# Kernel optimization log

Hardware: AMD Instinct MI355X
Metric: run time of the kernel (lower is better)

The kernel has to match this reference:

```python
import jax, jax.numpy as jnp
import numpy as np

D_MODEL = 2048
D_FF = 8192
EPS = 1e-5


def layernorm(x, g, b):
    m = x.mean(-1, keepdims=True)
    v = ((x - m) ** 2).mean(-1, keepdims=True)
    return (x - m) * jax.lax.rsqrt(v + EPS) * g + b


def rotate_half(x):
    return jnp.concatenate([-x[..., ::2], x[..., 1::2]], axis=-1)


def sinu_pos_emb(dim, length):
    inv_freq = 1.0 / 10000 ** (jnp.arange(0, dim, 2, dtype=jnp.float32) / dim)
    pos = jnp.arange(length, dtype=jnp.float32)
    sp = pos[:, None] * inv_freq[None, :]           # [S, dim/2]
    return jnp.concatenate([jnp.sin(sp), jnp.cos(sp)], axis=-1)  # [S, dim]


def setup_inputs() -> dict:
    key = jax.random.key(0)
    ks = jax.random.split(key, 10)
    d, f = D_MODEL, D_FF
    sc = 0.02
    return {
        "src":  jax.random.normal(ks[0], (4, 2048, d), jnp.float32),
        "Wqkv": jax.random.normal(ks[1], (3 * d, d), jnp.float32) * sc,
        "bqkv": jnp.zeros((3 * d,), jnp.float32),
        "Wo":   jax.random.normal(ks[2], (d, d), jnp.float32) * sc,
        "bo":   jnp.zeros((d,), jnp.float32),
        "W1":   jax.random.normal(ks[3], (f, d), jnp.float32) * sc,
        "b1":   jnp.zeros((f,), jnp.float32),
        "W2":   jax.random.normal(ks[4], (d, f), jnp.float32) * sc,
        "b2":   jnp.zeros((d,), jnp.float32),
        "g1":   jnp.ones((d,), jnp.float32),
        "be1":  jnp.zeros((d,), jnp.float32),
        "g2":   jnp.ones((d,), jnp.float32),
        "be2":  jnp.zeros((d,), jnp.float32),
    }


def reference(src, Wqkv, bqkv, Wo, bo, W1, b1, W2, b2, g1, be1, g2, be2):
    B, S, d = src.shape
    # norm1 (note: torch code reassigns src, so residuals use the normed value)
    src = layernorm(src, g1, be1)
    qkv = src @ Wqkv.T + bqkv                      # [B,S,3d]
    Q, K, V = qkv[..., :d], qkv[..., d:2 * d], qkv[..., 2 * d:]
    # rotary: cos/sin of the (sin,cos)-concatenated table, faithful to source
    emb = sinu_pos_emb(d, S)                       # [S,d]
    c, s = jnp.cos(emb), jnp.sin(emb)
    Q = Q * c + rotate_half(Q) * s
    K = K * c - rotate_half(K) * s
    # causal SDPA over full d_model (no head split in source)
    scale = 1.0 / jnp.sqrt(jnp.float32(d))
    scores = jnp.einsum('bqd,bkd->bqk', Q, K) * scale
    causal = jnp.tril(jnp.ones((S, S), bool))
    scores = jnp.where(causal, scores, jnp.float32(-1e30))
    P = jax.nn.softmax(scores, axis=-1)
    attn = jnp.einsum('bqk,bkd->bqd', P, V)
    src = src + attn @ Wo.T + bo
    # FFN block
    h = layernorm(src, g2, be2)
    h = jax.nn.relu(h @ W1.T + b1) @ W2.T + b2
    return src + h
```

## Files before the change

kernel.cpp:

```cpp
#include <hip/hip_runtime.h>
#include <cstdint>


typedef __attribute__((ext_vector_type(8))) short short8;
typedef __attribute__((ext_vector_type(4))) float floatx4;

#define PLANE 16777216L
#define SS    4194304L

__device__ __forceinline__ float bf2f(unsigned short u) {
    union { unsigned int i; float f; } v; v.i = ((unsigned int)u) << 16; return v.f;
}
__device__ __forceinline__ unsigned short f2bf(float f) {
    union { float f; unsigned int i; } v; v.f = f;
    unsigned int x = v.i;
    return (unsigned short)((x + 0x7FFFu + ((x >> 16) & 1u)) >> 16);
}
__device__ __forceinline__ uint4 pack8(float4 a, float4 b) {
    unsigned short o[8];
    o[0] = f2bf(a.x); o[1] = f2bf(a.y); o[2] = f2bf(a.z); o[3] = f2bf(a.w);
    o[4] = f2bf(b.x); o[5] = f2bf(b.y); o[6] = f2bf(b.z); o[7] = f2bf(b.w);
    return *(uint4*)o;
}
__device__ __forceinline__ void gl_lds16(const void* g, void* l) {
    __builtin_amdgcn_global_load_lds(
        (const __attribute__((address_space(1))) void*)g,
        (__attribute__((address_space(3))) void*)l, 16, 0, 0);
}

#define EM_QKV  0
#define EM_SC   1
#define EM_PV   2
#define EM_PROJ 3
#define EM_FFN1 4
#define EM_F2A  5

template<int EM>
__launch_bounds__(256, 2)
__global__ void gemm_bt(const unsigned short* __restrict__ A,
                        const unsigned short* __restrict__ B,
                        void* __restrict__ Cv, int N, int K,
                        const float* __restrict__ bias,
                        const unsigned short* __restrict__ resid16,
                        unsigned short* __restrict__ outQ,
                        unsigned short* __restrict__ outVt)
{
    constexpr int BM = 128, BN = 128, BK = 32;
    __shared__ __align__(16) unsigned short As[BM * BK];
    __shared__ __align__(16) unsigned short Bs[BN * BK];

    const int m0 = blockIdx.x * BM, n0 = blockIdx.y * BN;
    if (EM == EM_SC && n0 > m0 + (BM - 1)) return;

    int kmax = K;
    if (EM == EM_PV) { kmax = m0 + BM; if (kmax > K) kmax = K; }
    const int nsteps = kmax / BK;

    const int t = threadIdx.x;
    const int lane = t & 63, wave = t >> 6;
    const int q = lane >> 4, ln = lane & 15;
    const int wm = (wave >> 1) * 64, wn = (wave & 1) * 64;

    const int r0 = wave * 32;
    const int rA = r0 + (lane >> 2);
    const int cslot = lane & 3;
    const int cg0 = (cslot ^ (rA & 3)) * 8;
    const int cg1 = (cslot ^ ((rA + 16) & 3)) * 8;
    const unsigned short* Agp0 = A + (long)(m0 + rA) * K + cg0;
    const unsigned short* Agp1 = A + (long)(m0 + rA + 16) * K + cg1;
    const unsigned short* Bgp0 = B + (long)(n0 + rA) * K + cg0;
    const unsigned short* Bgp1 = B + (long)(n0 + rA + 16) * K + cg1;
    unsigned short* lA0 = &As[r0 * 32];
    unsigned short* lA1 = &As[(r0 + 16) * 32];
    unsigned short* lB0 = &Bs[r0 * 32];
    unsigned short* lB1 = &Bs[(r0 + 16) * 32];

    floatx4 acc[4][4];
#pragma unroll
    for (int i = 0; i < 4; ++i)
#pragma unroll
        for (int j = 0; j < 4; ++j) acc[i][j] = (floatx4){0.f, 0.f, 0.f, 0.f};

    for (int s = 0; s < nsteps; ++s) {
        const long off = (long)s * BK;
        __syncthreads();
        gl_lds16(Agp0 + off, lA0);
        gl_lds16(Agp1 + off, lA1);
        gl_lds16(Bgp0 + off, lB0);
        gl_lds16(Bgp1 + off, lB1);
        __syncthreads();
        short8 af[4], bfr[4];
#pragma unroll
        for (int i = 0; i < 4; ++i) {
            const int R = wm + 16 * i + ln;
            af[i] = *(const short8*)&As[R * 32 + ((q ^ (R & 3)) * 8)];
        }
#pragma unroll
        for (int j = 0; j < 4; ++j) {
            const int R = wn + 16 * j + ln;
            bfr[j] = *(const short8*)&Bs[R * 32 + ((q ^ (R & 3)) * 8)];
        }
#pragma unroll
        for (int i = 0; i < 4; ++i)
#pragma unroll
            for (int j = 0; j < 4; ++j)
                acc[i][j] = __builtin_amdgcn_mfma_f32_16x16x32_bf16(af[i], bfr[j], acc[i][j], 0, 0, 0);
    }

#pragma unroll
    for (int i = 0; i < 4; ++i) {
#pragma unroll
        for (int r = 0; r < 4; ++r) {
            const int row = m0 + wm + 16 * i + q * 4 + r;
#pragma unroll
            for (int j = 0; j < 4; ++j) {
                const int col = n0 + wn + 16 * j + ln;
                float v = acc[i][j][r];
                const long idx = (long)row * N + col;
                if constexpr (EM == EM_SC) {
                    ((unsigned short*)Cv)[idx] = f2bf(v);
                } else if constexpr (EM == EM_PV) {
                    ((unsigned short*)Cv)[idx] = f2bf(v);
                }
            }
        }
    }
}

#define BAR()    __builtin_amdgcn_s_barrier()
#define LGKM0()  asm volatile("s_waitcnt lgkmcnt(0)" ::: "memory")
#define VMCNT(n) asm volatile("s_waitcnt vmcnt(" #n ")" ::: "memory")

template<int EM>
__launch_bounds__(512, 2)
__global__ void gemm256(const unsigned short* __restrict__ A,
                        const unsigned short* __restrict__ B,
                        void* __restrict__ Cv, int N, int K,
                        const float* __restrict__ bias,
                        const unsigned short* __restrict__ resid16,
                        unsigned short* __restrict__ outQ,
                        unsigned short* __restrict__ outVt)
{
    __shared__ __align__(16) unsigned short As[2][16384];
    __shared__ __align__(16) unsigned short Bs[2][16384];

    const int m0 = blockIdx.x * 256, n0 = blockIdx.y * 256;
    const int t = threadIdx.x;
    const int lane = t & 63, wave = t >> 6;
    const int q = lane >> 4, ln = lane & 15;
    const int wm = wave >> 2, wn = wave & 3;

    const int jrow = lane >> 3;
    const int csrc = ((lane & 7) ^ jrow) * 8;
    const unsigned short* Ag = A + (long)(m0 + wave * 16 + jrow) * K + csrc;
    const unsigned short* Bg = B + (long)(n0 + wave * 16 + jrow) * K + csrc;
    const int ldsSlice = wave * 1024;

    const int aBase = (wm * 128 + ln) * 64;
    const int bBase = (wn * 64 + ln) * 64;
    const int c0 = ((0 + q) ^ (ln & 7)) * 8;
    const int c1 = ((4 + q) ^ (ln & 7)) * 8;

    floatx4 acc[8][4];
#pragma unroll
    for (int i = 0; i < 8; ++i)
#pragma unroll
        for (int j = 0; j < 4; ++j) acc[i][j] = (floatx4){0.f, 0.f, 0.f, 0.f};

    short8 a[4][2];
    short8 b[2][2][2];

#define STAGE_A(buf, kt, h) do { \
    const unsigned short* _g = Ag + (long)((h) * 128) * K + ((long)(kt) << 6); \
    gl_lds16(_g,          &As[buf][(h) * 8192 + ldsSlice]); \
    gl_lds16(_g + 8L * K, &As[buf][(h) * 8192 + ldsSlice + 512]); \
} while (0)
#define STAGE_B(buf, kt, h) do { \
    const unsigned short* _g = Bg + (long)((h) * 128) * K + ((long)(kt) << 6); \
    gl_lds16(_g,          &Bs[buf][(h) * 8192 + ldsSlice]); \
    gl_lds16(_g + 8L * K, &Bs[buf][(h) * 8192 + ldsSlice + 512]); \
} while (0)
#define RD_A(sel, mg) { \
    _Pragma("unroll") \
    for (int i = 0; i < 4; ++i) { \
        a[i][0] = *(const short8*)&As[sel][aBase + ((mg) * 64 + 16 * i) * 64 + c0]; \
        a[i][1] = *(const short8*)&As[sel][aBase + ((mg) * 64 + 16 * i) * 64 + c1]; \
    } }
#define RD_B(sel, ng) { \
    _Pragma("unroll") \
    for (int j = 0; j < 2; ++j) { \
        b[ng][j][0] = *(const short8*)&Bs[sel][bBase + ((ng) * 32 + 16 * j) * 64 + c0]; \
        b[ng][j][1] = *(const short8*)&Bs[sel][bBase + ((ng) * 32 + 16 * j) * 64 + c1]; \
    } }
#define MM(mg, ng) { \
    _Pragma("unroll") \
    for (int i = 0; i < 4; ++i) \
    _Pragma("unroll") \
    for (int j = 0; j < 2; ++j) { \
        acc[(mg)*4+i][(ng)*2+j] = __builtin_amdgcn_mfma_f32_16x16x32_bf16( \
            a[i][0], b[ng][j][0], acc[(mg)*4+i][(ng)*2+j], 0, 0, 0); \
        acc[(mg)*4+i][(ng)*2+j] = __builtin_amdgcn_mfma_f32_16x16x32_bf16( \
            a[i][1], b[ng][j][1], acc[(mg)*4+i][(ng)*2+j], 0, 0, 0); \
    } }

    const int nIter = K >> 7;

    STAGE_A(0, 0, 0); STAGE_A(0, 0, 1);
    STAGE_B(0, 0, 0); STAGE_B(0, 0, 1);
    STAGE_B(1, 1, 0); STAGE_B(1, 1, 1);
    VMCNT(4); BAR();

    for (int it = 0; it < nIter - 1; ++it) {
        const int k1 = 2 * it + 1, ke = 2 * it + 2, ko = 2 * it + 3;
        RD_A(0, 0); RD_B(0, 0);
        STAGE_A(1, k1, 0);
        BAR(); LGKM0();
        __builtin_amdgcn_s_setprio(1); MM(0, 0); __builtin_amdgcn_s_setprio(0);
        BAR();
        RD_B(0, 1);
        STAGE_A(1, k1, 1);
        BAR(); LGKM0();
        __builtin_amdgcn_s_setprio(1); MM(0, 1); __builtin_amdgcn_s_setprio(0);
        BAR();
        RD_A(0, 1);
        STAGE_B(0, ke, 0);
        BAR(); LGKM0();
        __builtin_amdgcn_s_setprio(1); MM(1, 0); __builtin_amdgcn_s_setprio(0);
        BAR();
        STAGE_B(0, ke, 1);
        BAR();
        __builtin_amdgcn_s_setprio(1); MM(1, 1); __builtin_amdgcn_s_setprio(0);
        VMCNT(4); BAR();
        RD_A(1, 0); RD_B(1, 0);
        STAGE_A(0, ke, 0);
        BAR(); LGKM0();
        __builtin_amdgcn_s_setprio(1); MM(0, 0); __builtin_amdgcn_s_setprio(0);
        BAR();
        RD_B(1, 1);
        STAGE_A(0, ke, 1);
        BAR(); LGKM0();
        __builtin_amdgcn_s_setprio(1); MM(0, 1); __builtin_amdgcn_s_setprio(0);
        BAR();
        RD_A(1, 1);
        STAGE_B(1, ko, 0);
        BAR(); LGKM0();
        __builtin_amdgcn_s_setprio(1); MM(1, 0); __builtin_amdgcn_s_setprio(0);
        BAR();
        STAGE_B(1, ko, 1);
        BAR();
        __builtin_amdgcn_s_setprio(1); MM(1, 1); __builtin_amdgcn_s_setprio(0);
        VMCNT(4); BAR();
    }

    {
        const int k1 = 2 * nIter - 1;
        RD_A(0, 0); RD_B(0, 0);
        STAGE_A(1, k1, 0);
        BAR(); LGKM0();
        __builtin_amdgcn_s_setprio(1); MM(0, 0); __builtin_amdgcn_s_setprio(0);
        BAR();
        RD_B(0, 1);
        STAGE_A(1, k1, 1);
        BAR(); LGKM0();
        __builtin_amdgcn_s_setprio(1); MM(0, 1); __builtin_amdgcn_s_setprio(0);
        BAR();
        RD_A(0, 1);
        BAR(); LGKM0();
        __builtin_amdgcn_s_setprio(1); MM(1, 0); __builtin_amdgcn_s_setprio(0);
        BAR();
        __builtin_amdgcn_s_setprio(1); MM(1, 1); __builtin_amdgcn_s_setprio(0);
        VMCNT(0); BAR();
        RD_A(1, 0); RD_B(1, 0);
        MM(0, 0);
        RD_B(1, 1);
        MM(0, 1);
        RD_A(1, 1);
        MM(1, 0); MM(1, 1);
    }

#undef STAGE_A
#undef STAGE_B
#undef RD_A
#undef RD_B
#undef MM

#pragma unroll
    for (int i = 0; i < 8; ++i) {
#pragma unroll
        for (int r = 0; r < 4; ++r) {
            const int row = m0 + wm * 128 + 16 * i + q * 4 + r;
#pragma unroll
            for (int j = 0; j < 4; ++j) {
                const int col = n0 + wn * 64 + 16 * j + ln;
                float v = acc[i][j][r];
                const long idx = (long)row * N + col;
                if constexpr (EM == EM_QKV) {
                    v += bias[col];
                    const unsigned short vb = f2bf(v);
                    const int p = col >> 11, c2 = col & 2047;
                    if (p == 0)      outQ[(long)row * 2048 + c2] = vb;
                    else if (p == 1) (outQ + PLANE)[(long)row * 2048 + c2] = vb;
                    else             outVt[(long)(row >> 11) * SS + (long)c2 * 2048 + (row & 2047)] = vb;
                } else if constexpr (EM == EM_PROJ) {
                    v += bias[col] + bf2f(resid16[idx]);
                    ((float*)Cv)[idx] = v;
                } else if constexpr (EM == EM_FFN1) {
                    v = fmaxf(v + bias[col], 0.f);
                    ((unsigned short*)Cv)[idx] = f2bf(v);
                } else {
                    ((float*)Cv)[idx] += v;
                }
            }
        }
    }
}

__launch_bounds__(256)
__global__ void cvt_rows(const float* __restrict__ src, unsigned short* __restrict__ dst, long srcld)
{
    const int row = blockIdx.x, t = threadIdx.x;
    const float* s = src + (long)row * srcld + t * 8;
    float4 a = *(const float4*)s;
    float4 b = *(const float4*)(s + 4);
    *(uint4*)(dst + (long)row * 2048 + t * 8) = pack8(a, b);
}

__launch_bounds__(256)
__global__ void layernorm_k(const float* __restrict__ X, unsigned short* __restrict__ Y,
                            const float* __restrict__ g, const float* __restrict__ be)
{
    const int row = blockIdx.x, t = threadIdx.x;
    const float* Xr = X + (long)row * 2048 + t * 8;
    float4 v0 = *(const float4*)Xr;
    float4 v1 = *(const float4*)(Xr + 4);
    float x[8] = {v0.x, v0.y, v0.z, v0.w, v1.x, v1.y, v1.z, v1.w};
    float s = 0.f, ss = 0.f;
#pragma unroll
    for (int k = 0; k < 8; ++k) { s += x[k]; ss += x[k] * x[k]; }
    for (int off = 32; off; off >>= 1) { s += __shfl_down(s, off, 64); ss += __shfl_down(ss, off, 64); }
    __shared__ float red[8];
    const int wave = t >> 6, lane = t & 63;
    if (lane == 0) { red[wave] = s; red[4 + wave] = ss; }
    __syncthreads();
    s  = red[0] + red[1] + red[2] + red[3];
    ss = red[4] + red[5] + red[6] + red[7];
    const float mean = s * (1.f / 2048.f);
    const float var  = ss * (1.f / 2048.f) - mean * mean;
    const float rstd = rsqrtf(var + 1e-5f);
    unsigned short o[8];
#pragma unroll
    for (int k = 0; k < 8; ++k) {
        const int col = t * 8 + k;
        o[k] = f2bf((x[k] - mean) * rstd * g[col] + be[col]);
    }
    *(uint4*)(Y + (long)row * 2048 + t * 8) = *(uint4*)o;
}

__launch_bounds__(256)
__global__ void rope_inplace(unsigned short* __restrict__ Q, unsigned short* __restrict__ K)
{
    __shared__ __align__(16) unsigned short rowbuf[2048];
    const int row = blockIdx.x;
    const int mtx = blockIdx.y;
    unsigned short* X = (mtx ? K : Q) + (long)row * 2048;
    const int t = threadIdx.x;
    *(uint4*)&rowbuf[t * 8] = *(const uint4*)(X + t * 8);
    __syncthreads();
    const int p = row & 2047;
    const float sgn = mtx ? -1.f : 1.f;
    unsigned short o[8];
#pragma unroll
    for (int e = 0; e < 8; ++e) {
        const int j = t * 8 + e;
        const int i = j & 1023;
        const float freq = __expf(-(float)i * (9.210340371976184f / 1024.0f));
        const float sp = (float)p * freq;
        const float emb = (j < 1024) ? sinf(sp) : cosf(sp);
        float se, ce;
        sincosf(emb, &se, &ce);
        const int pj = (j < 1024) ? (2 * j) : (2 * j - 2047);
        float xp = bf2f(rowbuf[pj]);
        if (j < 1024) xp = -xp;
        o[e] = f2bf(bf2f(rowbuf[j]) * ce + sgn * xp * se);
    }
    *(uint4*)(X + t * 8) = *(uint4*)o;
}

__launch_bounds__(256)
__global__ void softmax_causal(unsigned short* __restrict__ S)
{
    const int qq = blockIdx.x;
    const int L = qq + 1;
    unsigned short* srow = S + (long)qq * 2048;
    const int t = threadIdx.x;
    const float scale = 0.022097086912079608f;
    float vals[8];
    float m = -1e30f;
#pragma unroll
    for (int u = 0; u < 8; ++u) {
        const int i2 = t + 256 * u;
        vals[u] = (i2 < L) ? bf2f(srow[i2]) * scale : -1e30f;
        m = fmaxf(m, vals[u]);
    }
    for (int off = 32; off; off >>= 1) m = fmaxf(m, __shfl_down(m, off, 64));
    __shared__ float red[8];
    const int wave = t >> 6, lane = t & 63;
    if (lane == 0) red[wave] = m;
    __syncthreads();
    m = fmaxf(fmaxf(red[0], red[1]), fmaxf(red[2], red[3]));
    float sum = 0.f;
#pragma unroll
    for (int u = 0; u < 8; ++u) {
        float e = __expf(vals[u] - m);
        e = (t + 256 * u < L) ? e : 0.f;
        vals[u] = e; sum += e;
    }
    for (int off = 32; off; off >>= 1) sum += __shfl_down(sum, off, 64);
    if (lane == 0) red[4 + wave] = sum;
    __syncthreads();
    sum = red[4] + red[5] + red[6] + red[7];
    const float inv = 1.0f / sum;
#pragma unroll
    for (int u = 0; u < 8; ++u) srow[t + 256 * u] = f2bf(vals[u] * inv);
}

__launch_bounds__(256)
__global__ void final_add(float* __restrict__ io, const float* __restrict__ b2)
{
    const int row = blockIdx.x, t = threadIdx.x;
    const long base = (long)row * 2048 + t * 8;
    float4 a0 = *(const float4*)(io + base);
    float4 a1 = *(const float4*)(io + base + 4);
    float4 c0 = *(const float4*)(b2 + t * 8);
    float4 c1 = *(const float4*)(b2 + t * 8 + 4);
    a0.x += c0.x; a0.y += c0.y; a0.z += c0.z; a0.w += c0.w;
    a1.x += c1.x; a1.y += c1.y; a1.z += c1.z; a1.w += c1.w;
    *(float4*)(io + base) = a0;
    *(float4*)(io + base + 4) = a1;
}

extern "C" void kernel_launch(void* const* d_in, const int* in_sizes, int n_in,
                              void* d_out, int out_size, void* d_ws, size_t ws_size,
                              hipStream_t stream)
{
    const float* src  = (const float*)d_in[0];
    const float* Wqkv = (const float*)d_in[1];
    const float* bqkv = (const float*)d_in[2];
    const float* Wo   = (const float*)d_in[3];
    const float* bo   = (const float*)d_in[4];
    const float* W1   = (const float*)d_in[5];
    const float* b1   = (const float*)d_in[6];
    const float* W2   = (const float*)d_in[7];
    const float* b2   = (const float*)d_in[8];
    const float* g1   = (const float*)d_in[9];
    const float* be1  = (const float*)d_in[10];
    const float* g2   = (const float*)d_in[11];
    const float* be2  = (const float*)d_in[12];

    char* ws = (char*)d_ws;
    const long MB = 1LL << 20;
    unsigned short* x1    = (unsigned short*)ws;
    unsigned short* Vt    = (unsigned short*)(ws + 32 * MB);
    unsigned short* Wqbf  = (unsigned short*)(ws + 64 * MB);
    unsigned short* attn  = (unsigned short*)(ws + 64 * MB);
    unsigned short* scP   = (unsigned short*)(ws + 96 * MB);
    unsigned short* Wobf  = (unsigned short*)(ws + 96 * MB);
    unsigned short* W1c   = (unsigned short*)(ws + 96 * MB);
    unsigned short* W2c   = (unsigned short*)(ws + 104 * MB);
    unsigned short* h2    = x1;
    unsigned short* f1    = Vt;

    unsigned short* Q    = (unsigned short*)d_out;
    float*          src2 = (float*)d_out;
    float*          out  = (float*)d_out;

    const dim3 blk(256);
    const dim3 blk512(512);

    cvt_rows<<<6144, blk, 0, stream>>>(Wqkv, Wqbf, 2048);
    layernorm_k<<<8192, blk, 0, stream>>>(src, x1, g1, be1);
    gemm256<EM_QKV><<<dim3(32, 24), blk512, 0, stream>>>(
        x1, Wqbf, nullptr, 6144, 2048, bqkv, nullptr, Q, Vt);
    rope_inplace<<<dim3(8192, 2), blk, 0, stream>>>(Q, Q + PLANE);

    for (int b = 0; b < 4; ++b) {
        gemm_bt<EM_SC><<<dim3(16, 16), blk, 0, stream>>>(
            Q + b * SS, Q + PLANE + b * SS, scP, 2048, 2048, nullptr, nullptr, nullptr, nullptr);
        softmax_causal<<<2048, blk, 0, stream>>>(scP);
        gemm_bt<EM_PV><<<dim3(16, 16), blk, 0, stream>>>(
            scP, Vt + b * SS, attn + b * SS, 2048, 2048, nullptr, nullptr, nullptr, nullptr);
    }

    cvt_rows<<<2048, blk, 0, stream>>>(Wo, Wobf, 2048);
    gemm256<EM_PROJ><<<dim3(32, 8), blk512, 0, stream>>>(
        attn, Wobf, src2, 2048, 2048, bo, x1, nullptr, nullptr);
    layernorm_k<<<8192, blk, 0, stream>>>(src2, h2, g2, be2);

    for (int c = 0; c < 4; ++c) {
        cvt_rows<<<2048, blk, 0, stream>>>(W1 + (long)c * 2048 * 2048, W1c, 2048);
        cvt_rows<<<2048, blk, 0, stream>>>(W2 + (long)c * 2048, W2c, 8192);
        gemm256<EM_FFN1><<<dim3(32, 8), blk512, 0, stream>>>(
            h2, W1c, f1, 2048, 2048, b1 + c * 2048, nullptr, nullptr, nullptr);
        gemm256<EM_F2A><<<dim3(32, 8), blk512, 0, stream>>>(
            f1, W2c, src2, 2048, 2048, nullptr, nullptr, nullptr, nullptr);
    }
    final_add<<<8192, blk, 0, stream>>>(out, b2);
}
```

Baseline: 1.527 ms.

## Restructure 256x256 GEMM main loop with split register fragments and partial lgkm waits

Rewrites the GEMM k-loop of the 256x256 MFMA kernel to iterate per 64-wide K-group with a ping-pong LDS schedule. Separate register fragment sets for the two M and N halves let LDS reads for the next quadrant be issued while the current quadrant's MFMAs run. Full lgkmcnt(0) waits become partial waits, and roughly half the barriers per stage are removed. The goal is better overlap of LDS reads and global-to-LDS staging with matrix math, at the cost of more live registers and more delicate wait counts that could race or spill.

Result: slower. 1.660 ms (+8.7%).

```diff
diff --git a/kernel.cpp b/kernel.cpp
--- a/kernel.cpp
+++ b/kernel.cpp
@@ -127,9 +127,11 @@
     }
 }
 
-#define BAR()    __builtin_amdgcn_s_barrier()
-#define LGKM0()  asm volatile("s_waitcnt lgkmcnt(0)" ::: "memory")
+#define BARM()   do { __builtin_amdgcn_s_barrier(); asm volatile("" ::: "memory"); } while (0)
+#define LGKM(n)  asm volatile("s_waitcnt lgkmcnt(" #n ")" ::: "memory")
 #define VMCNT(n) asm volatile("s_waitcnt vmcnt(" #n ")" ::: "memory")
+#define PRIO1()  __builtin_amdgcn_s_setprio(1)
+#define PRIO0()  __builtin_amdgcn_s_setprio(0)
 
 template<int EM>
 __launch_bounds__(512, 2)
@@ -167,8 +169,8 @@
 #pragma unroll
         for (int j = 0; j < 4; ++j) acc[i][j] = (floatx4){0.f, 0.f, 0.f, 0.f};
 
-    short8 a[4][2];
-    short8 b[2][2][2];
+    short8 a0r[4][2], a1r[4][2];
+    short8 b0r[2][2], b1r[2][2];
 
 #define STAGE_A(buf, kt, h) do { \
     const unsigned short* _g = Ag + (long)((h) * 128) * K + ((long)(kt) << 6); \
@@ -180,109 +182,107 @@
     gl_lds16(_g,          &Bs[buf][(h) * 8192 + ldsSlice]); \
     gl_lds16(_g + 8L * K, &Bs[buf][(h) * 8192 + ldsSlice + 512]); \
 } while (0)
-#define RD_A(sel, mg) { \
-    _Pragma("unroll") \
-    for (int i = 0; i < 4; ++i) { \
-        a[i][0] = *(const short8*)&As[sel][aBase + ((mg) * 64 + 16 * i) * 64 + c0]; \
-        a[i][1] = *(const short8*)&As[sel][aBase + ((mg) * 64 + 16 * i) * 64 + c1]; \
-    } }
-#define RD_B(sel, ng) { \
+#define RD_A0F(sel, i) { \
+    a0r[i][0] = *(const short8*)&As[sel][aBase + (16 * (i)) * 64 + c0]; \
+    a0r[i][1] = *(const short8*)&As[sel][aBase + (16 * (i)) * 64 + c1]; }
+#define RD_A1F(sel, i) { \
+    a1r[i][0] = *(const short8*)&As[sel][aBase + (64 + 16 * (i)) * 64 + c0]; \
+    a1r[i][1] = *(const short8*)&As[sel][aBase + (64 + 16 * (i)) * 64 + c1]; }
+#define RD_B0A(sel) { \
     _Pragma("unroll") \
     for (int j = 0; j < 2; ++j) { \
-        b[ng][j][0] = *(const short8*)&Bs[sel][bBase + ((ng) * 32 + 16 * j) * 64 + c0]; \
-        b[ng][j][1] = *(const short8*)&Bs[sel][bBase + ((ng) * 32 + 16 * j) * 64 + c1]; \
-    } }
-#define MM(mg, ng) { \
+        b0r[j][0] = *(const short8*)&Bs[sel][bBase + (16 * j) * 64 + c0]; \
+        b0r[j][1] = *(const short8*)&Bs[sel][bBase + (16 * j) * 64 + c1]; } }
+#define RD_B1A(sel) { \
+    _Pragma("unroll") \
+    for (int j = 0; j < 2; ++j) { \
+        b1r[j][0] = *(const short8*)&Bs[sel][bBase + (32 + 16 * j) * 64 + c0]; \
+        b1r[j][1] = *(const short8*)&Bs[sel][bBase + (32 + 16 * j) * 64 + c1]; } }
+#define MMQ(ar, br, mg, ng) { \
     _Pragma("unroll") \
     for (int i = 0; i < 4; ++i) \
     _Pragma("unroll") \
     for (int j = 0; j < 2; ++j) { \
         acc[(mg)*4+i][(ng)*2+j] = __builtin_amdgcn_mfma_f32_16x16x32_bf16( \
-            a[i][0], b[ng][j][0], acc[(mg)*4+i][(ng)*2+j], 0, 0, 0); \
+            ar[i][0], br[j][0], acc[(mg)*4+i][(ng)*2+j], 0, 0, 0); \
         acc[(mg)*4+i][(ng)*2+j] = __builtin_amdgcn_mfma_f32_16x16x32_bf16( \
-            a[i][1], b[ng][j][1], acc[(mg)*4+i][(ng)*2+j], 0, 0, 0); \
+            ar[i][1], br[j][1], acc[(mg)*4+i][(ng)*2+j], 0, 0, 0); \
     } }
 
-    const int nIter = K >> 7;
+    const int NG = K >> 6;
 
     STAGE_A(0, 0, 0); STAGE_A(0, 0, 1);
     STAGE_B(0, 0, 0); STAGE_B(0, 0, 1);
-    STAGE_B(1, 1, 0); STAGE_B(1, 1, 1);
-    VMCNT(4); BAR();
-
-    for (int it = 0; it < nIter - 1; ++it) {
-        const int k1 = 2 * it + 1, ke = 2 * it + 2, ko = 2 * it + 3;
-        RD_A(0, 0); RD_B(0, 0);
-        STAGE_A(1, k1, 0);
-        BAR(); LGKM0();
-        __builtin_amdgcn_s_setprio(1); MM(0, 0); __builtin_amdgcn_s_setprio(0);
-        BAR();
-        RD_B(0, 1);
-        STAGE_A(1, k1, 1);
-        BAR(); LGKM0();
-        __builtin_amdgcn_s_setprio(1); MM(0, 1); __builtin_amdgcn_s_setprio(0);
-        BAR();
-        RD_A(0, 1);
-        STAGE_B(0, ke, 0);
-        BAR(); LGKM0();
-        __builtin_amdgcn_s_setprio(1); MM(1, 0); __builtin_amdgcn_s_setprio(0);
-        BAR();
-        STAGE_B(0, ke, 1);
-        BAR();
-        __builtin_amdgcn_s_setprio(1); MM(1, 1); __builtin_amdgcn_s_setprio(0);
-        VMCNT(4); BAR();
-        RD_A(1, 0); RD_B(1, 0);
-        STAGE_A(0, ke, 0);
-        BAR(); LGKM0();
-        __builtin_amdgcn_s_setprio(1); MM(0, 0); __builtin_amdgcn_s_setprio(0);
-        BAR();
-        RD_B(1, 1);
-        STAGE_A(0, ke, 1);
-        BAR(); LGKM0();
-        __builtin_amdgcn_s_setprio(1); MM(0, 1); __builtin_amdgcn_s_setprio(0);
-        BAR();
-        RD_A(1, 1);
-        STAGE_B(1, ko, 0);
-        BAR(); LGKM0();
-        __builtin_amdgcn_s_setprio(1); MM(1, 0); __builtin_amdgcn_s_setprio(0);
-        BAR();
-        STAGE_B(1, ko, 1);
-        BAR();
-        __builtin_amdgcn_s_setprio(1); MM(1, 1); __builtin_amdgcn_s_setprio(0);
-        VMCNT(4); BAR();
-    }
-
+    STAGE_B(1, 1, 0);
+    STAGE_A(1, 1, 0);
+    VMCNT(4); BARM();
+    RD_A0F(0, 0); RD_A0F(0, 1); RD_A0F(0, 2); RD_A0F(0, 3);
+    RD_B0A(0);
+
+    for (int g = 0; g < NG - 2; ++g) {
+        const int cur = g & 1, nxt = cur ^ 1;
+        RD_B1A(cur); RD_A1F(cur, 0);
+        STAGE_A(nxt, g + 1, 1);
+        LGKM(6);
+        PRIO1(); MMQ(a0r, b0r, 0, 0); PRIO0();
+        BARM();
+        RD_A1F(cur, 1); RD_A1F(cur, 2); RD_A1F(cur, 3);
+        STAGE_B(nxt, g + 1, 1);
+        LGKM(6);
+        PRIO1(); MMQ(a0r, b1r, 0, 1); PRIO0();
+        VMCNT(2); BARM();
+        RD_A0F(nxt, 0); RD_A0F(nxt, 1); RD_A0F(nxt, 2);
+        STAGE_B(cur, g + 2, 0);
+        LGKM(6);
+        PRIO1(); MMQ(a1r, b0r, 1, 0); PRIO0();
+        VMCNT(2); BARM();
+        RD_A0F(nxt, 3); RD_B0A(nxt);
+        STAGE_A(cur, g + 2, 0);
+        LGKM(6);
+        PRIO1(); MMQ(a1r, b1r, 1, 1); PRIO0();
+        BARM();
+    }
     {
-        const int k1 = 2 * nIter - 1;
-        RD_A(0, 0); RD_B(0, 0);
-        STAGE_A(1, k1, 0);
-        BAR(); LGKM0();
-        __builtin_amdgcn_s_setprio(1); MM(0, 0); __builtin_amdgcn_s_setprio(0);
-        BAR();
-        RD_B(0, 1);
-        STAGE_A(1, k1, 1);
-        BAR(); LGKM0();
-        __builtin_amdgcn_s_setprio(1); MM(0, 1); __builtin_amdgcn_s_setprio(0);
-        BAR();
-        RD_A(0, 1);
-        BAR(); LGKM0();
-        __builtin_amdgcn_s_setprio(1); MM(1, 0); __builtin_amdgcn_s_setprio(0);
-        BAR();
-        __builtin_amdgcn_s_setprio(1); MM(1, 1); __builtin_amdgcn_s_setprio(0);
-        VMCNT(0); BAR();
-        RD_A(1, 0); RD_B(1, 0);
-        MM(0, 0);
-        RD_B(1, 1);
-        MM(0, 1);
-        RD_A(1, 1);
-        MM(1, 0); MM(1, 1);
+        const int g = NG - 2, cur = g & 1, nxt = cur ^ 1;
+        RD_B1A(cur); RD_A1F(cur, 0);
+        STAGE_A(nxt, g + 1, 1);
+        LGKM(6);
+        PRIO1(); MMQ(a0r, b0r, 0, 0); PRIO0();
+        BARM();
+        RD_A1F(cur, 1); RD_A1F(cur, 2); RD_A1F(cur, 3);
+        STAGE_B(nxt, g + 1, 1);
+        LGKM(6);
+        PRIO1(); MMQ(a0r, b1r, 0, 1); PRIO0();
+        VMCNT(2); BARM();
+        RD_A0F(nxt, 0); RD_A0F(nxt, 1); RD_A0F(nxt, 2);
+        LGKM(6);
+        PRIO1(); MMQ(a1r, b0r, 1, 0); PRIO0();
+        VMCNT(0); BARM();
+        RD_A0F(nxt, 3); RD_B0A(nxt);
+        LGKM(6);
+        PRIO1(); MMQ(a1r, b1r, 1, 1); PRIO0();
+        BARM();
+    }
+    {
+        const int cur = (NG - 1) & 1;
+        RD_B1A(cur); RD_A1F(cur, 0);
+        LGKM(6);
+        PRIO1(); MMQ(a0r, b0r, 0, 0); PRIO0();
+        RD_A1F(cur, 1); RD_A1F(cur, 2); RD_A1F(cur, 3);
+        LGKM(6);
+        PRIO1(); MMQ(a0r, b1r, 0, 1); PRIO0();
+        LGKM(0);
+        PRIO1(); MMQ(a1r, b0r, 1, 0); PRIO0();
+        PRIO1(); MMQ(a1r, b1r, 1, 1); PRIO0();
     }
 
 #undef STAGE_A
 #undef STAGE_B
-#undef RD_A
-#undef RD_B
-#undef MM
+#undef RD_A0F
+#undef RD_A1F
+#undef RD_B0A
+#undef RD_B1A
+#undef MMQ
 
 #pragma unroll
     for (int i = 0; i < 8; ++i) {
```

## Batch attention kernels over two batches per launch and hoist W1 conversion

Applied to the files above, without the earlier changes.

Attention score, softmax and PV GEMMs now process two batch elements per launch via a z grid dimension and per-batch strides, halving the launch count and doubling the grid size to fill more CUs. The LDS swizzle is changed to XOR with (row>>1)&3 to cut bank conflicts on fragment reads. W1 is converted to bf16 once into a larger buffer instead of per chunk. The scores buffer now holds two 2048x2048 planes, which needs more workspace.

Result: faster. 1.370 ms (-10.3%).

```diff
diff --git a/kernel.cpp b/kernel.cpp
--- a/kernel.cpp
+++ b/kernel.cpp
@@ -40,14 +40,16 @@
 __global__ void gemm_bt(const unsigned short* __restrict__ A,
                         const unsigned short* __restrict__ B,
                         void* __restrict__ Cv, int N, int K,
-                        const float* __restrict__ bias,
-                        const unsigned short* __restrict__ resid16,
-                        unsigned short* __restrict__ outQ,
-                        unsigned short* __restrict__ outVt)
+                        long zA, long zB, long zC)
 {
     constexpr int BM = 128, BN = 128, BK = 32;
     __shared__ __align__(16) unsigned short As[BM * BK];
     __shared__ __align__(16) unsigned short Bs[BN * BK];
+
+    const int z = blockIdx.z;
+    A += (long)z * zA;
+    B += (long)z * zB;
+    unsigned short* C16 = (unsigned short*)Cv + (long)z * zC;
 
     const int m0 = blockIdx.x * BM, n0 = blockIdx.y * BN;
     if (EM == EM_SC && n0 > m0 + (BM - 1)) return;
@@ -64,8 +66,8 @@
     const int r0 = wave * 32;
     const int rA = r0 + (lane >> 2);
     const int cslot = lane & 3;
-    const int cg0 = (cslot ^ (rA & 3)) * 8;
-    const int cg1 = (cslot ^ ((rA + 16) & 3)) * 8;
+    const int cg0 = (cslot ^ ((rA >> 1) & 3)) * 8;
+    const int cg1 = (cslot ^ (((rA + 16) >> 1) & 3)) * 8;
     const unsigned short* Agp0 = A + (long)(m0 + rA) * K + cg0;
     const unsigned short* Agp1 = A + (long)(m0 + rA + 16) * K + cg1;
     const unsigned short* Bgp0 = B + (long)(n0 + rA) * K + cg0;
@@ -93,12 +95,12 @@
 #pragma unroll
         for (int i = 0; i < 4; ++i) {
             const int R = wm + 16 * i + ln;
-            af[i] = *(const short8*)&As[R * 32 + ((q ^ (R & 3)) * 8)];
+            af[i] = *(const short8*)&As[R * 32 + ((q ^ ((R >> 1) & 3)) * 8)];
         }
 #pragma unroll
         for (int j = 0; j < 4; ++j) {
             const int R = wn + 16 * j + ln;
-            bfr[j] = *(const short8*)&Bs[R * 32 + ((q ^ (R & 3)) * 8)];
+            bfr[j] = *(const short8*)&Bs[R * 32 + ((q ^ ((R >> 1) & 3)) * 8)];
         }
 #pragma unroll
         for (int i = 0; i < 4; ++i)
@@ -115,13 +117,8 @@
 #pragma unroll
             for (int j = 0; j < 4; ++j) {
                 const int col = n0 + wn + 16 * j + ln;
-                float v = acc[i][j][r];
                 const long idx = (long)row * N + col;
-                if constexpr (EM == EM_SC) {
-                    ((unsigned short*)Cv)[idx] = f2bf(v);
-                } else if constexpr (EM == EM_PV) {
-                    ((unsigned short*)Cv)[idx] = f2bf(v);
-                }
+                C16[idx] = f2bf(acc[i][j][r]);
             }
         }
     }
@@ -391,7 +388,7 @@
 {
     const int qq = blockIdx.x;
     const int L = qq + 1;
-    unsigned short* srow = S + (long)qq * 2048;
+    unsigned short* srow = S + (long)blockIdx.y * SS + (long)qq * 2048;
     const int t = threadIdx.x;
     const float scale = 0.022097086912079608f;
     float vals[8];
@@ -463,9 +460,9 @@
     unsigned short* Vt    = (unsigned short*)(ws + 32 * MB);
     unsigned short* Wqbf  = (unsigned short*)(ws + 64 * MB);
     unsigned short* attn  = (unsigned short*)(ws + 64 * MB);
+    unsigned short* W1bf  = (unsigned short*)(ws + 64 * MB);
     unsigned short* scP   = (unsigned short*)(ws + 96 * MB);
     unsigned short* Wobf  = (unsigned short*)(ws + 96 * MB);
-    unsigned short* W1c   = (unsigned short*)(ws + 96 * MB);
     unsigned short* W2c   = (unsigned short*)(ws + 104 * MB);
     unsigned short* h2    = x1;
     unsigned short* f1    = Vt;
@@ -483,12 +480,13 @@
         x1, Wqbf, nullptr, 6144, 2048, bqkv, nullptr, Q, Vt);
     rope_inplace<<<dim3(8192, 2), blk, 0, stream>>>(Q, Q + PLANE);
 
-    for (int b = 0; b < 4; ++b) {
-        gemm_bt<EM_SC><<<dim3(16, 16), blk, 0, stream>>>(
-            Q + b * SS, Q + PLANE + b * SS, scP, 2048, 2048, nullptr, nullptr, nullptr, nullptr);
-        softmax_causal<<<2048, blk, 0, stream>>>(scP);
-        gemm_bt<EM_PV><<<dim3(16, 16), blk, 0, stream>>>(
-            scP, Vt + b * SS, attn + b * SS, 2048, 2048, nullptr, nullptr, nullptr, nullptr);
+    for (int p = 0; p < 2; ++p) {
+        const long b0 = 2L * p;
+        gemm_bt<EM_SC><<<dim3(16, 16, 2), blk, 0, stream>>>(
+            Q + b0 * SS, Q + PLANE + b0 * SS, scP, 2048, 2048, SS, SS, SS);
+        softmax_causal<<<dim3(2048, 2), blk, 0, stream>>>(scP);
+        gemm_bt<EM_PV><<<dim3(16, 16, 2), blk, 0, stream>>>(
+            scP, Vt + b0 * SS, attn + b0 * SS, 2048, 2048, SS, SS, SS);
     }
 
     cvt_rows<<<2048, blk, 0, stream>>>(Wo, Wobf, 2048);
@@ -496,11 +494,11 @@
         attn, Wobf, src2, 2048, 2048, bo, x1, nullptr, nullptr);
     layernorm_k<<<8192, blk, 0, stream>>>(src2, h2, g2, be2);
 
+    cvt_rows<<<8192, blk, 0, stream>>>(W1, W1bf, 2048);
     for (int c = 0; c < 4; ++c) {
-        cvt_rows<<<2048, blk, 0, stream>>>(W1 + (long)c * 2048 * 2048, W1c, 2048);
         cvt_rows<<<2048, blk, 0, stream>>>(W2 + (long)c * 2048, W2c, 8192);
         gemm256<EM_FFN1><<<dim3(32, 8), blk512, 0, stream>>>(
-            h2, W1c, f1, 2048, 2048, b1 + c * 2048, nullptr, nullptr, nullptr);
+            h2, W1bf + (long)c * SS, f1, 2048, 2048, b1 + c * 2048, nullptr, nullptr, nullptr);
         gemm256<EM_F2A><<<dim3(32, 8), blk512, 0, stream>>>(
             f1, W2c, src2, 2048, 2048, nullptr, nullptr, nullptr, nullptr);
     }
```
